# Optimization experiments

Measured on AMD Instinct MI355X. Metric: run time of the kernel, lower is better.

The kernel has to match this reference:

```python
import jax, jax.numpy as jnp
import numpy as np

EPS = 1e-12
NEG = -1e30


def setup_inputs() -> dict:
    key = jax.random.key(0)
    ks = jax.random.split(key, 7)
    B, Nq, Lp, H, D = 96, 35, 180, 768, 128
    q_hidden = jax.random.normal(ks[0], (B, Nq, H), dtype=jnp.float32)
    pos_hidden = jax.random.normal(ks[1], (B, Lp, H), dtype=jnp.float32)
    neg_hidden = jax.random.normal(ks[2], (B, Lp, H), dtype=jnp.float32)
    W = jax.random.normal(ks[3], (H, D), dtype=jnp.float32) * 0.02
    b = jax.random.normal(ks[4], (D,), dtype=jnp.float32) * 0.02
    # non-punctuation filter mask; guarantee at least one valid token per passage
    pos_mask = jax.random.bernoulli(ks[5], 0.85, (B, Lp)).at[:, 0].set(True)
    neg_mask = jax.random.bernoulli(ks[6], 0.85, (B, Lp)).at[:, 0].set(True)
    return {"q_hidden": q_hidden, "pos_hidden": pos_hidden, "neg_hidden": neg_hidden,
            "W": W, "b": b, "pos_mask": pos_mask, "neg_mask": neg_mask}


def _vector_representation(h, W, b):
    # Linear projection then F.normalize(x) with torch default dim=1,
    # i.e. normalization over the SEQUENCE axis (faithful to source).
    x = jnp.einsum('blh,hd->bld', h, W) + b
    norm = jnp.maximum(jnp.sqrt(jnp.sum(x * x, axis=1, keepdims=True)), EPS)
    return x / norm


def _late_interaction(q, p, mask):
    # q: [Bq, Nq, D], p: [Bp, Lp, D], mask: [Bp, Lp] (True = keep token)
    sim = jnp.einsum('qnd,pld->qpnl', q, p)          # [Bq, Bp, Nq, Lp]
    sim = jnp.where(mask[None, :, None, :], sim, NEG)
    return jnp.max(sim, axis=-1).sum(axis=-1)        # MaxSim: max over Lp, sum over Nq


def reference(q_hidden, pos_hidden, neg_hidden, W, b, pos_mask, neg_mask):
    q = _vector_representation(q_hidden, W, b)
    pos = _vector_representation(pos_hidden, W, b)
    neg = _vector_representation(neg_hidden, W, b)
    pos_scores = _late_interaction(q, pos, pos_mask)
    neg_scores = _late_interaction(q, neg, neg_mask)
    return jnp.concatenate((pos_scores, neg_scores), axis=1)  # [B, 2B]
```

## Files before the change

### kernel.cpp

```cpp
#include <hip/hip_runtime.h>

typedef __attribute__((ext_vector_type(4))) float f32x4;
typedef __attribute__((ext_vector_type(8))) short s16x8;
typedef __attribute__((ext_vector_type(4))) short s16x4;
typedef __bf16 bf16x4 __attribute__((ext_vector_type(4)));

#define B_   96
#define NQ   35
#define LP   180
#define H_   768
#define D_   128
#define NEGF (-1e30f)

#define NROWS 37920
#define QROWS 3360
#define PROWS 17280

__device__ __forceinline__ unsigned short f2bf(float f) {
    return __builtin_bit_cast(unsigned short, (__bf16)f);
}

__device__ __forceinline__ void cvt_hilo(f32x4 v0, f32x4 v1, s16x8* hi, s16x8* lo) {
    bf16x4 h0 = __builtin_convertvector(v0, bf16x4);
    bf16x4 h1 = __builtin_convertvector(v1, bf16x4);
    f32x4 r0 = v0 - __builtin_convertvector(h0, f32x4);
    f32x4 r1 = v1 - __builtin_convertvector(h1, f32x4);
    bf16x4 l0 = __builtin_convertvector(r0, bf16x4);
    bf16x4 l1 = __builtin_convertvector(r1, bf16x4);
    s16x4 h0s = __builtin_bit_cast(s16x4, h0), h1s = __builtin_bit_cast(s16x4, h1);
    s16x4 l0s = __builtin_bit_cast(s16x4, l0), l1s = __builtin_bit_cast(s16x4, l1);
    *hi = __builtin_shufflevector(h0s, h1s, 0, 1, 2, 3, 4, 5, 6, 7);
    *lo = __builtin_shufflevector(l0s, l1s, 0, 1, 2, 3, 4, 5, 6, 7);
}

__global__ __launch_bounds__(256) void prep_k(
    const float* __restrict__ W, unsigned short* __restrict__ wthi,
    const unsigned int* __restrict__ pmask_w, unsigned int* __restrict__ ctrl,
    float* __restrict__ ssq) {
    __shared__ unsigned int rr[256];
    int b = blockIdx.x, t = threadIdx.x;
    if (b < 48) {
        int tid = b * 256 + t;
        int nt = tid / (24 * 64);
        int r = tid - nt * 24 * 64;
        int ks = r / 64, lane = r - ks * 64;
        int m = lane & 15, quad = lane >> 4;
        unsigned short* o = wthi + (size_t)tid * 8;
#pragma unroll
        for (int j = 0; j < 8; j++) {
            int k = ks * 32 + quad * 8 + j;
            o[j] = f2bf(W[(size_t)k * D_ + nt * 16 + m]);
        }
    } else if (b < 192) {
        ssq[(b - 48) * 256 + t] = 0.f;
    } else {
        unsigned int f1 = 0, f3 = 0, f4 = 0;
        for (int w = t; w < 4320; w += 256) {
            unsigned int v = pmask_w[w];
            f1 |= v & 0x0000ff00u;
            f3 |= v & 0xff000000u;
            if (w & 1) f4 |= v & 0x000000ffu;
        }
        rr[t] = f1; __syncthreads();
        for (int s2 = 128; s2; s2 >>= 1) { if (t < s2) rr[t] |= rr[t + s2]; __syncthreads(); }
        if (!t) ctrl[0] = rr[0];
        __syncthreads();
        rr[t] = f3; __syncthreads();
        for (int s2 = 128; s2; s2 >>= 1) { if (t < s2) rr[t] |= rr[t + s2]; __syncthreads(); }
        if (!t) ctrl[1] = rr[0];
        __syncthreads();
        rr[t] = f4; __syncthreads();
        for (int s2 = 128; s2; s2 >>= 1) { if (t < s2) rr[t] |= rr[t + s2]; __syncthreads(); }
        if (!t) ctrl[2] = rr[0];
    }
}

__global__ __launch_bounds__(256) void proj_k(
    const float* __restrict__ qh, const float* __restrict__ ph, const float* __restrict__ nh,
    const unsigned short* __restrict__ wthi, const float* __restrict__ bias,
    float* __restrict__ x, float* __restrict__ ssq,
    const void* __restrict__ pm, const void* __restrict__ nm,
    const unsigned int* __restrict__ ctrl, unsigned char* __restrict__ maskc) {
    __shared__ f32x4 part[4][8][64];
    int b = blockIdx.x;
    if (b >= 2370) {
        int i = (b - 2370) * 256 + threadIdx.x;
        const void* src = (i < B_ * LP) ? pm : nm;
        int j = (i < B_ * LP) ? i : i - B_ * LP;
        unsigned int c1 = ctrl[0], c3 = ctrl[1], c4 = ctrl[2];
        bool bit;
        if (c1 > 0)       bit = ((const unsigned char*)src)[j] != 0;
        else if (c3 > 0)  bit = ((const float*)src)[j] != 0.0f;
        else if (c4 > 0)  bit = ((const int*)src)[j] != 0;
        else              bit = ((const long long*)src)[j] != 0;
        maskc[i] = bit ? 1 : 0;
        return;
    }
    int wave = threadIdx.x >> 6, lane = threadIdx.x & 63;
    int rg = b;
    const float* src; int row0l; int growbase;
    if (rg < 210)       { src = qh; row0l = rg * 16;          growbase = row0l; }
    else if (rg < 1290) { src = ph; row0l = (rg - 210) * 16;  growbase = QROWS + row0l; }
    else                { src = nh; row0l = (rg - 1290) * 16; growbase = QROWS + PROWS + row0l; }
    int m = lane & 15, quad = lane >> 4;
    const float* ap = src + (size_t)(row0l + m) * H_ + wave * 192 + quad * 8;

    f32x4 acc[8];
#pragma unroll
    for (int nt = 0; nt < 8; nt++) acc[nt] = (f32x4){0.f, 0.f, 0.f, 0.f};

#pragma unroll 2
    for (int kl = 0; kl < 6; kl++) {
        const f32x4* pA = (const f32x4*)(ap + kl * 32);
        f32x4 v0 = pA[0], v1 = pA[1];
        s16x8 ahi, alo;
        cvt_hilo(v0, v1, &ahi, &alo);
        int ksg = wave * 6 + kl;
        s16x8 bh[8];
#pragma unroll
        for (int nt = 0; nt < 8; nt++)
            bh[nt] = *(const s16x8*)(wthi + ((size_t)(nt * 24 + ksg) * 64 + lane) * 8);
#pragma unroll
        for (int nt = 0; nt < 8; nt++) {
            acc[nt] = __builtin_amdgcn_mfma_f32_16x16x32_bf16(ahi, bh[nt], acc[nt], 0, 0, 0);
            acc[nt] = __builtin_amdgcn_mfma_f32_16x16x32_bf16(alo, bh[nt], acc[nt], 0, 0, 0);
        }
    }
#pragma unroll
    for (int nt = 0; nt < 8; nt++) part[wave][nt][lane] = acc[nt];
    __syncthreads();

    int bk0, bk1, b1start;
    if (growbase < QROWS)              { bk0 = growbase / 35;  bk1 = (growbase + 15) / 35;
                                         b1start = bk1 * 35; }
    else if (growbase < QROWS + PROWS) { int r0 = growbase - QROWS;
                                         bk0 = 96 + r0 / 180;  bk1 = 96 + (r0 + 15) / 180;
                                         b1start = QROWS + (bk1 - 96) * 180; }
    else                               { int r0 = growbase - QROWS - PROWS;
                                         bk0 = 192 + r0 / 180; bk1 = 192 + (r0 + 15) / 180;
                                         b1start = QROWS + PROWS + (bk1 - 192) * 180; }

#pragma unroll
    for (int q2 = 0; q2 < 2; q2++) {
        int nt = wave * 2 + q2;
        f32x4 s = part[0][nt][lane];
        s += part[1][nt][lane];
        s += part[2][nt][lane];
        s += part[3][nt][lane];
        int col = nt * 16 + m;
        float bv = bias[col];
        float slo = 0.f, shi = 0.f;
#pragma unroll
        for (int r = 0; r < 4; r++) {
            int grow = growbase + quad * 4 + r;
            float v = s[r] + bv;
            x[(size_t)grow * D_ + col] = v;
            float v2 = v * v;
            if (bk1 > bk0 && grow >= b1start) shi += v2; else slo += v2;
        }
        slo += __shfl_xor(slo, 16); slo += __shfl_xor(slo, 32);
        if (quad == 0) atomicAdd(ssq + (size_t)bk0 * D_ + col, slo);
        if (bk1 > bk0) {
            shi += __shfl_xor(shi, 16); shi += __shfl_xor(shi, 32);
            if (quad == 0) atomicAdd(ssq + (size_t)bk1 * D_ + col, shi);
        }
    }
}

__global__ __launch_bounds__(256) void scatter_k(
    const float* __restrict__ x, const float* __restrict__ ssq,
    const unsigned char* __restrict__ maskc,
    unsigned short* __restrict__ qfrag, unsigned short* __restrict__ pfrag) {
    int idx = blockIdx.x * 256 + threadIdx.x;
    if (idx < QROWS * D_) {
        int row = idx >> 7, d = idx & 127;
        int ks = d >> 5, quad = (d >> 3) & 3, j = d & 7;
        int b = row / 35, l = row - b * 35;
        int qp = b >> 1, prow = (b & 1) * 35 + l;
        int mt = prow >> 4, mm = prow & 15;
        float iv = rsqrtf(fmaxf(ssq[(size_t)b * D_ + d], 1e-24f));
        float v = x[idx] * iv;
        qfrag[(((size_t)((qp * 5 + mt) * 4 + ks) * 64 + quad * 16 + mm) * 8 + j)] = f2bf(v);
    } else {
        int t = idx - QROWS * D_;
        int d = t & 127;
        int u = t >> 7;
        int l = u % 192, pbk = u / 192;
        int ks = d >> 5, quad = (d >> 3) & 3, j = d & 7;
        int lsrc = (l < LP && maskc[pbk * LP + l]) ? l : 0;
        size_t o = (QROWS + (size_t)pbk * LP + lsrc) * D_ + d;
        float iv = rsqrtf(fmaxf(ssq[(size_t)(96 + pbk) * D_ + d], 1e-24f));
        float v = x[o] * iv;
        int nt = l >> 4, mm = l & 15;
        pfrag[(((size_t)(pbk * 12 + nt) * 4 + ks) * 64 + quad * 16 + mm) * 8 + j] = f2bf(v);
    }
}

__global__ __launch_bounds__(256, 3) void interact_k(
    const unsigned short* __restrict__ qfrag, const unsigned short* __restrict__ pfrag,
    float* __restrict__ out) {
    int wave = threadIdx.x >> 6, lane = threadIdx.x & 63;
    int b = blockIdx.x;
    int xcd = b & 7, i = b >> 3;
    int c = xcd * 24 + (i % 24);
    int qg = i / 24;
    int side = c / 96, pb = c - side * 96;
    int qp = qg * 4 + wave;
    int m = lane & 15, quad = lane >> 4;

    const unsigned short* pbase = pfrag + (size_t)c * 24576;
    const unsigned short* qbase = qfrag + (size_t)qp * 10240;

    s16x8 a[5][4];
#pragma unroll
    for (int mt = 0; mt < 5; mt++)
#pragma unroll
        for (int ks = 0; ks < 4; ks++)
            a[mt][ks] = *(const s16x8*)(qbase + ((size_t)(mt * 4 + ks) * 64 + lane) * 8);

    const f32x4 zero4 = (f32x4){0.f, 0.f, 0.f, 0.f};
    float rmax[5][4];
#pragma unroll
    for (int mt = 0; mt < 5; mt++)
#pragma unroll
        for (int rr = 0; rr < 4; rr++) rmax[mt][rr] = NEGF;

    for (int nt = 0; nt < 12; nt++) {
        s16x8 bfr[4];
#pragma unroll
        for (int ks = 0; ks < 4; ks++)
            bfr[ks] = *(const s16x8*)(pbase + ((size_t)(nt * 4 + ks) * 64 + lane) * 8);
#pragma unroll
        for (int mt = 0; mt < 5; mt++) {
            f32x4 acc = __builtin_amdgcn_mfma_f32_16x16x32_bf16(a[mt][0], bfr[0], zero4, 0, 0, 0);
            acc = __builtin_amdgcn_mfma_f32_16x16x32_bf16(a[mt][1], bfr[1], acc, 0, 0, 0);
            acc = __builtin_amdgcn_mfma_f32_16x16x32_bf16(a[mt][2], bfr[2], acc, 0, 0, 0);
            acc = __builtin_amdgcn_mfma_f32_16x16x32_bf16(a[mt][3], bfr[3], acc, 0, 0, 0);
#pragma unroll
            for (int rr = 0; rr < 4; rr++)
                rmax[mt][rr] = fmaxf(rmax[mt][rr], acc[rr]);
        }
    }

#pragma unroll
    for (int mt = 0; mt < 5; mt++)
#pragma unroll
        for (int rr = 0; rr < 4; rr++) {
            float v = rmax[mt][rr];
            v = fmaxf(v, __shfl_xor(v, 1));
            v = fmaxf(v, __shfl_xor(v, 2));
            v = fmaxf(v, __shfl_xor(v, 4));
            v = fmaxf(v, __shfl_xor(v, 8));
            rmax[mt][rr] = v;
        }
    float s0 = 0.f, s1 = 0.f;
#pragma unroll
    for (int mt = 0; mt < 5; mt++)
#pragma unroll
        for (int rr = 0; rr < 4; rr++) {
            int prow = mt * 16 + quad * 4 + rr;
            float v = rmax[mt][rr];
            if (prow < 35) s0 += v;
            else if (prow < 70) s1 += v;
        }
    s0 += __shfl_xor(s0, 16); s0 += __shfl_xor(s0, 32);
    s1 += __shfl_xor(s1, 16); s1 += __shfl_xor(s1, 32);
    if (lane == 0) {
        int qb0 = qp * 2, qb1 = qp * 2 + 1;
        out[(size_t)qb0 * (2 * B_) + side * B_ + pb] = s0;
        out[(size_t)qb1 * (2 * B_) + side * B_ + pb] = s1;
    }
}

extern "C" void kernel_launch(void* const* d_in, const int* in_sizes, int n_in,
                              void* d_out, int out_size, void* d_ws, size_t ws_size,
                              hipStream_t stream) {
    const float* qh   = (const float*)d_in[0];
    const float* ph   = (const float*)d_in[1];
    const float* nh   = (const float*)d_in[2];
    const float* W    = (const float*)d_in[3];
    const float* bias = (const float*)d_in[4];
    const void* pmask = d_in[5];
    const void* nmask = d_in[6];
    float* out = (float*)d_out;
    char* ws = (char*)d_ws;

    constexpr size_t CTRL_OFF  = 0;
    constexpr size_t WTHI_OFF  = 256;
    constexpr size_t MASKC_OFF = WTHI_OFF + 196608;
    constexpr size_t SSQ_OFF   = 231424;
    constexpr size_t X_OFF     = SSQ_OFF + 147456;
    constexpr size_t QFRAG_OFF = X_OFF + (size_t)NROWS * D_ * 4;
    constexpr size_t PFRAG_OFF = QFRAG_OFF + 983040;

    unsigned int* ctrl     = (unsigned int*)(ws + CTRL_OFF);
    unsigned short* wthi   = (unsigned short*)(ws + WTHI_OFF);
    unsigned char* maskc   = (unsigned char*)(ws + MASKC_OFF);
    float* ssq             = (float*)(ws + SSQ_OFF);
    float* x               = (float*)(ws + X_OFF);
    unsigned short* qfrag  = (unsigned short*)(ws + QFRAG_OFF);
    unsigned short* pfrag  = (unsigned short*)(ws + PFRAG_OFF);

    prep_k<<<193, 256, 0, stream>>>(W, wthi, (const unsigned int*)pmask, ctrl, ssq);
    proj_k<<<2370 + 135, 256, 0, stream>>>(qh, ph, nh, wthi, bias, x, ssq,
                                           pmask, nmask, ctrl, maskc);
    scatter_k<<<20112, 256, 0, stream>>>(x, ssq, maskc, qfrag, pfrag);
    interact_k<<<2304, 256, 0, stream>>>(qfrag, pfrag, out);
}
```

Before: 218.7 us.

## Vectorize scatter to one 8-element fragment per thread, prefetch A in proj

The scatter kernel now gives each thread one full 8-element bf16 MFMA fragment. It reads x and ssq with 16-byte vector loads and writes a single 16-byte store, replacing per-element scalar loads and 2-byte scattered stores, and cuts the grid by 8x. The projection kernel loads all six A-tile slices up front before the MFMA loop, so global-load latency is exposed once instead of per iteration, at the cost of more registers. The query padding rows (prow>=70) are now written explicitly as zeros.

```diff
diff --git a/kernel.cpp b/kernel.cpp
--- a/kernel.cpp
+++ b/kernel.cpp
@@ -31,6 +31,13 @@
     s16x4 l0s = __builtin_bit_cast(s16x4, l0), l1s = __builtin_bit_cast(s16x4, l1);
     *hi = __builtin_shufflevector(h0s, h1s, 0, 1, 2, 3, 4, 5, 6, 7);
     *lo = __builtin_shufflevector(l0s, l1s, 0, 1, 2, 3, 4, 5, 6, 7);
+}
+
+__device__ __forceinline__ s16x8 pack_bf16(f32x4 v0, f32x4 v1) {
+    bf16x4 h0 = __builtin_convertvector(v0, bf16x4);
+    bf16x4 h1 = __builtin_convertvector(v1, bf16x4);
+    s16x4 a = __builtin_bit_cast(s16x4, h0), b = __builtin_bit_cast(s16x4, h1);
+    return __builtin_shufflevector(a, b, 0, 1, 2, 3, 4, 5, 6, 7);
 }
 
 __global__ __launch_bounds__(256) void prep_k(
@@ -105,16 +112,22 @@
     int m = lane & 15, quad = lane >> 4;
     const float* ap = src + (size_t)(row0l + m) * H_ + wave * 192 + quad * 8;
 
-    f32x4 acc[8];
-#pragma unroll
-    for (int nt = 0; nt < 8; nt++) acc[nt] = (f32x4){0.f, 0.f, 0.f, 0.f};
-
-#pragma unroll 2
+    f32x4 av[12];
+#pragma unroll
     for (int kl = 0; kl < 6; kl++) {
         const f32x4* pA = (const f32x4*)(ap + kl * 32);
-        f32x4 v0 = pA[0], v1 = pA[1];
+        av[2 * kl]     = pA[0];
+        av[2 * kl + 1] = pA[1];
+    }
+
+    f32x4 acc[8];
+#pragma unroll
+    for (int nt = 0; nt < 8; nt++) acc[nt] = (f32x4){0.f, 0.f, 0.f, 0.f};
+
+#pragma unroll
+    for (int kl = 0; kl < 6; kl++) {
         s16x8 ahi, alo;
-        cvt_hilo(v0, v1, &ahi, &alo);
+        cvt_hilo(av[2 * kl], av[2 * kl + 1], &ahi, &alo);
         int ksg = wave * 6 + kl;
         s16x8 bh[8];
 #pragma unroll
@@ -171,28 +184,51 @@
     const float* __restrict__ x, const float* __restrict__ ssq,
     const unsigned char* __restrict__ maskc,
     unsigned short* __restrict__ qfrag, unsigned short* __restrict__ pfrag) {
-    int idx = blockIdx.x * 256 + threadIdx.x;
-    if (idx < QROWS * D_) {
-        int row = idx >> 7, d = idx & 127;
-        int ks = d >> 5, quad = (d >> 3) & 3, j = d & 7;
-        int b = row / 35, l = row - b * 35;
-        int qp = b >> 1, prow = (b & 1) * 35 + l;
-        int mt = prow >> 4, mm = prow & 15;
-        float iv = rsqrtf(fmaxf(ssq[(size_t)b * D_ + d], 1e-24f));
-        float v = x[idx] * iv;
-        qfrag[(((size_t)((qp * 5 + mt) * 4 + ks) * 64 + quad * 16 + mm) * 8 + j)] = f2bf(v);
+    int c = blockIdx.x * 256 + threadIdx.x;
+    int lane = c & 63, ks = (c >> 6) & 3;
+    int quad = lane >> 4, mm = lane & 15;
+    int d0 = ks * 32 + quad * 8;
+    if (c < 61440) {
+        int g = c >> 8;
+        int mt = g % 5, qp = g / 5;
+        int prow = mt * 16 + mm;
+        s16x8 outv = (s16x8){0, 0, 0, 0, 0, 0, 0, 0};
+        if (prow < 70) {
+            int hi = prow >= 35;
+            int bq = qp * 2 + hi;
+            int l = prow - hi * 35;
+            size_t row = (size_t)bq * 35 + l;
+            const f32x4* px = (const f32x4*)(x + row * D_ + d0);
+            f32x4 v0 = px[0], v1 = px[1];
+            const f32x4* pq = (const f32x4*)(ssq + (size_t)bq * D_ + d0);
+            f32x4 q0 = pq[0], q1 = pq[1];
+            f32x4 r0, r1;
+#pragma unroll
+            for (int j = 0; j < 4; j++) {
+                r0[j] = rsqrtf(fmaxf(q0[j], 1e-24f));
+                r1[j] = rsqrtf(fmaxf(q1[j], 1e-24f));
+            }
+            outv = pack_bf16(v0 * r0, v1 * r1);
+        }
+        *(s16x8*)(qfrag + (size_t)c * 8) = outv;
     } else {
-        int t = idx - QROWS * D_;
-        int d = t & 127;
-        int u = t >> 7;
-        int l = u % 192, pbk = u / 192;
-        int ks = d >> 5, quad = (d >> 3) & 3, j = d & 7;
+        int c2 = c - 61440;
+        int g = c2 >> 8;
+        int nt = g % 12, pbk = g / 12;
+        int l = nt * 16 + mm;
         int lsrc = (l < LP && maskc[pbk * LP + l]) ? l : 0;
-        size_t o = (QROWS + (size_t)pbk * LP + lsrc) * D_ + d;
-        float iv = rsqrtf(fmaxf(ssq[(size_t)(96 + pbk) * D_ + d], 1e-24f));
-        float v = x[o] * iv;
-        int nt = l >> 4, mm = l & 15;
-        pfrag[(((size_t)(pbk * 12 + nt) * 4 + ks) * 64 + quad * 16 + mm) * 8 + j] = f2bf(v);
+        size_t row = QROWS + (size_t)pbk * LP + lsrc;
+        const f32x4* px = (const f32x4*)(x + row * D_ + d0);
+        f32x4 v0 = px[0], v1 = px[1];
+        const f32x4* pq = (const f32x4*)(ssq + (size_t)(96 + pbk) * D_ + d0);
+        f32x4 q0 = pq[0], q1 = pq[1];
+        f32x4 r0, r1;
+#pragma unroll
+        for (int j = 0; j < 4; j++) {
+            r0[j] = rsqrtf(fmaxf(q0[j], 1e-24f));
+            r1[j] = rsqrtf(fmaxf(q1[j], 1e-24f));
+        }
+        *(s16x8*)(pfrag + (size_t)c2 * 8) = pack_bf16(v0 * r0, v1 * r1);
     }
 }
 
@@ -304,6 +340,6 @@
     prep_k<<<193, 256, 0, stream>>>(W, wthi, (const unsigned int*)pmask, ctrl, ssq);
     proj_k<<<2370 + 135, 256, 0, stream>>>(qh, ph, nh, wthi, bias, x, ssq,
                                            pmask, nmask, ctrl, maskc);
-    scatter_k<<<20112, 256, 0, stream>>>(x, ssq, maskc, qfrag, pfrag);
+    scatter_k<<<2544, 256, 0, stream>>>(x, ssq, maskc, qfrag, pfrag);
     interact_k<<<2304, 256, 0, stream>>>(qfrag, pfrag, out);
 }
```

Result: no change. 220.0 us (+0.6%).
